# Optimization experiments

Hardware: AMD Instinct MI355X
Metric: run time of the kernel (lower is better)

## Reference

```python
import jax, jax.numpy as jnp
import numpy as np

B, S, D = 64, 14, 2048   # batch, enc_image_size, encoder_dim
A, H, E = 512, 512, 512  # attention_dim, lstm_size, embedding_size
V, L = 10000, 20         # vocab_size, max caption length (T = L-1 decode steps)


def setup_inputs() -> dict:
    key = jax.random.key(0)
    ks = jax.random.split(key, 24)
    p = lambda k, shape: jax.random.normal(k, shape, jnp.float32) * 0.02
    features = jax.random.normal(ks[0], (B, S, S, D), jnp.float32)
    captions = jax.random.randint(ks[1], (B, L), 0, V)
    # sorted descending lengths in [2, L], max forced to L so T_dec = L-1
    lengths = jnp.sort(jax.random.randint(ks[2], (B,), 2, L + 1))[::-1]
    lengths = lengths.at[0].set(L)
    return {
        'features': features, 'captions': captions, 'lengths': lengths,
        'emb': p(ks[3], (V, E)),
        'W_ih': p(ks[4], (4 * H, D + E)), 'b_ih': p(ks[5], (4 * H,)),
        'W_hh': p(ks[6], (4 * H, H)), 'b_hh': p(ks[7], (4 * H,)),
        'h_fc_w': p(ks[8], (H, D)), 'h_fc_b': p(ks[9], (H,)),
        'c_fc_w': p(ks[10], (H, D)), 'c_fc_b': p(ks[11], (H,)),
        'f_beta_w': p(ks[12], (D, H)), 'f_beta_b': p(ks[13], (D,)),
        'cls_w': p(ks[14], (V, H)), 'cls_b': p(ks[15], (V,)),
        'enc_w': p(ks[16], (A, D)), 'enc_b': p(ks[17], (A,)),
        'dec_w': p(ks[18], (A, H)), 'dec_b': p(ks[19], (A,)),
        'att_w': p(ks[20], (1, A)), 'att_b': p(ks[21], (1,)),
    }


def reference(features, captions, lengths, emb, W_ih, b_ih, W_hh, b_hh,
              h_fc_w, h_fc_b, c_fc_w, c_fc_b, f_beta_w, f_beta_b,
              cls_w, cls_b, enc_w, enc_b, dec_w, dec_b, att_w, att_b):
    feats = features.reshape(features.shape[0], -1, features.shape[-1])  # (B,P,D)
    emb_seq = emb[captions]                                              # (B,L,E)
    mean_f = feats.mean(axis=1)
    h = mean_f @ h_fc_w.T + h_fc_b
    c = mean_f @ c_fc_w.T + c_fc_b
    dec_len = lengths - 1
    T = captions.shape[1] - 1
    # attention encoder projection is time-invariant: hoist out of the loop
    att1 = jnp.einsum('bpd,ad->bpa', feats, enc_w) + enc_b               # (B,P,A)

    def step(carry, xs):
        h, c = carry
        x_emb, t = xs
        att2 = h @ dec_w.T + dec_b                                       # (B,A)
        e = jnp.einsum('bpa,a->bp', jax.nn.relu(att1 + att2[:, None, :]), att_w[0]) + att_b[0]
        alpha = jax.nn.softmax(e, axis=1)                                # (B,P)
        awe = jnp.einsum('bp,bpd->bd', alpha, feats)
        gate = jax.nn.sigmoid(h @ f_beta_w.T + f_beta_b)
        awe = gate * awe
        x = jnp.concatenate([x_emb, awe], axis=1)                        # (B,E+D)
        gates = x @ W_ih.T + b_ih + h @ W_hh.T + b_hh                    # torch gate order i,f,g,o
        i, f, g, o = jnp.split(gates, 4, axis=1)
        c2 = jax.nn.sigmoid(f) * c + jax.nn.sigmoid(i) * jnp.tanh(g)
        h2 = jax.nn.sigmoid(o) * jnp.tanh(c2)
        y = h2 @ cls_w.T + cls_b                                         # dropout = eval identity
        active = (t < dec_len)[:, None]
        return (h2, c2), (jnp.where(active, y, 0.0), jnp.where(active, alpha, 0.0))

    xs = (jnp.swapaxes(emb_seq[:, :T], 0, 1), jnp.arange(T))
    (_, _), (y_pred, alphas) = jax.lax.scan(step, (h, c), xs)
    return jnp.swapaxes(y_pred, 0, 1), jnp.swapaxes(alphas, 0, 1)
```

## Files before the change

kernel.cpp:

```cpp
#include <hip/hip_runtime.h>
#include <math.h>

typedef __attribute__((ext_vector_type(8))) short bf16x8;
typedef __attribute__((ext_vector_type(8))) unsigned short u16x8;
typedef __attribute__((ext_vector_type(4))) float f32x4;

#define NB 64
#define NP 196
#define ND 2048
#define NA 512
#define NH 512
#define NE 512
#define NV 10000
#define NT 19
#define NKX 3072
#define NROW (NB*NP)
#define NVP 10112
#define MROW 1280
#define PP 200

__device__ __forceinline__ unsigned short f2bu(float f){
    unsigned int u; __builtin_memcpy(&u, &f, 4);
    u = (u + 0x7FFFu + ((u >> 16) & 1u)) >> 16;
    return (unsigned short)u;
}
__device__ __forceinline__ float b2f(short s){
    unsigned int u = ((unsigned int)(unsigned short)s) << 16;
    float f; __builtin_memcpy(&f, &u, 4); return f;
}
__device__ __forceinline__ float sigm(float x){ return 1.f/(1.f + __expf(-x)); }

__device__ __forceinline__ void gll16(const void* g, void* l){
    __builtin_amdgcn_global_load_lds(
        (const __attribute__((address_space(1))) void*)g,
        (__attribute__((address_space(3))) void*)l, 16, 0, 0);
}


__global__ void k_cast4(const float4* __restrict__ src, ushort4* __restrict__ dst, int n4){
    int stride = gridDim.x * blockDim.x;
    for (int i = blockIdx.x*blockDim.x + threadIdx.x; i < n4; i += stride){
        float4 v = src[i];
        ushort4 o = { f2bu(v.x), f2bu(v.y), f2bu(v.z), f2bu(v.w) };
        dst[i] = o;
    }
}

__global__ void k_wcat(const float* __restrict__ wih, const float* __restrict__ whh,
                       unsigned short* __restrict__ wcat){
    int j = blockIdx.x;
    int k = blockIdx.y*256 + threadIdx.x;
    float v = (k < 2560) ? wih[j*2560 + k] : whh[j*512 + (k - 2560)];
    wcat[j*NKX + k] = f2bu(v);
}

__global__ void k_tr(const float* __restrict__ feats,
                     unsigned short* __restrict__ fbf,
                     unsigned short* __restrict__ ftr,
                     float* __restrict__ meanf){
    __shared__ unsigned short sm[64][202];
    __shared__ float rsum[256];
    int dt = blockIdx.x;
    int b  = blockIdx.y;
    int tid = threadIdx.x;
    int d = tid & 63;
    int gd = dt*64 + d;
    float s = 0.f;
    for (int p = (tid >> 6); p < NP; p += 4){
        float v = feats[((size_t)(b*NP + p))*ND + gd];
        unsigned short u = f2bu(v);
        fbf[((size_t)(b*NP + p))*ND + gd] = u;
        sm[d][p] = u;
        s += v;
    }
    rsum[tid] = s;
    __syncthreads();
    if (tid < 64)
        meanf[b*ND + dt*64 + tid] =
            (rsum[tid] + rsum[tid+64] + rsum[tid+128] + rsum[tid+192]) * (1.f/196.f);
    for (int v = tid; v < 64*25; v += 256){
        int r = v/25, c = v - r*25;
        u16x8 o;
        #pragma unroll
        for (int j = 0; j < 8; j++){ int p = c*8 + j; o[j] = (p < NP) ? sm[r][p] : (unsigned short)0; }
        *(u16x8*)(ftr + ((size_t)(b*ND + dt*64 + r))*PP + c*8) = o;
    }
}

__global__ void k_hc0(const float* __restrict__ meanf,
                      const float* __restrict__ hw, const float* __restrict__ hb,
                      const float* __restrict__ cw, const float* __restrict__ cb,
                      unsigned short* __restrict__ hbf, float* __restrict__ cst){
    int sel = blockIdx.y;
    const float* wmat = sel ? cw : hw;
    const float* bias = sel ? cb : hb;
    int jg = blockIdx.x;
    int tid = threadIdx.x;
    int b = tid & 63, jj = tid >> 6;
    int j = jg*4 + jj;
    __shared__ float ml[64][33];
    __shared__ float wl[4][32];
    float acc = 0.f;
    for (int kc = 0; kc < ND; kc += 32){
        __syncthreads();
        #pragma unroll
        for (int q = 0; q < 8; q++){
            int lin = tid + q*256;
            int r = lin >> 5, kk = lin & 31;
            ml[r][kk] = meanf[r*ND + kc + kk];
        }
        if (tid < 128){ int r = tid >> 5, kk = tid & 31; wl[r][kk] = wmat[(jg*4 + r)*ND + kc + kk]; }
        __syncthreads();
        #pragma unroll
        for (int kk = 0; kk < 32; kk++) acc += ml[b][kk] * wl[jj][kk];
    }
    acc += bias[j];
    if (sel) cst[b*NH + j] = acc;
    else     hbf[b*NH + j] = f2bu(acc);
}

template<int K>
__device__ __forceinline__ void gemm128(const unsigned short* __restrict__ A,
                                        const unsigned short* __restrict__ B,
                                        int brow, int bcol, f32x4 acc[4][4]){
    __shared__ unsigned short As[128*32];
    __shared__ unsigned short Bs[128*32];
    int tid = threadIdx.x;
    int w = tid >> 6, l = tid & 63;
    int wr = (w >> 1) * 64, wc = (w & 1) * 64;
    int lr = l & 15, kg = (l >> 4) * 8;
    const unsigned short* ga0 = A + (size_t)(brow + (tid >> 2))*K + (tid & 3)*8;
    const unsigned short* gb0 = B + (size_t)(bcol + (tid >> 2))*K + (tid & 3)*8;
    for (int k0 = 0; k0 < K; k0 += 32){
        __syncthreads();
        gll16(ga0 + k0,            As + w*512);
        gll16(ga0 + (size_t)64*K + k0, As + 2048 + w*512);
        gll16(gb0 + k0,            Bs + w*512);
        gll16(gb0 + (size_t)64*K + k0, Bs + 2048 + w*512);
        __syncthreads();
        bf16x8 af[4], bfr[4];
        #pragma unroll
        for (int mi = 0; mi < 4; mi++)
            af[mi] = *(const bf16x8*)(As + (wr + mi*16 + lr)*32 + kg);
        #pragma unroll
        for (int ni = 0; ni < 4; ni++)
            bfr[ni] = *(const bf16x8*)(Bs + (wc + ni*16 + lr)*32 + kg);
        #pragma unroll
        for (int ni = 0; ni < 4; ni++){
            #pragma unroll
            for (int mi = 0; mi < 4; mi++)
                acc[mi][ni] = __builtin_amdgcn_mfma_f32_16x16x32_bf16(af[mi], bfr[ni], acc[mi][ni], 0, 0, 0);
        }
    }
}

__global__ void k_gemm_att1(const unsigned short* __restrict__ fbf,
                            const unsigned short* __restrict__ encw,
                            const float* __restrict__ enc_b,
                            unsigned short* __restrict__ att1){
    f32x4 acc[4][4] = {};
    int brow = blockIdx.x*128, bcol = blockIdx.y*128;
    gemm128<ND>(fbf, encw, brow, bcol, acc);
    int w = threadIdx.x >> 6, l = threadIdx.x & 63;
    int wr = (w >> 1) * 64, wc = (w & 1) * 64;
    int r0 = brow + wr + (l >> 4)*4;
    int c0 = bcol + wc + (l & 15);
    #pragma unroll
    for (int ni = 0; ni < 4; ni++){
        int col = c0 + ni*16;
        float eb = enc_b[col];
        #pragma unroll
        for (int mi = 0; mi < 4; mi++){
            #pragma unroll
            for (int r = 0; r < 4; r++)
                att1[(size_t)(r0 + mi*16 + r)*NA + col] = f2bu(acc[mi][ni][r] + eb);
        }
    }
}

__global__ void k_gemm_cls(const unsigned short* __restrict__ hsb,
                           const unsigned short* __restrict__ clsw,
                           const float* __restrict__ cls_b,
                           const int* __restrict__ lengths,
                           float* __restrict__ yout){
    f32x4 acc[4][4] = {};
    int brow = blockIdx.x*128, bcol = blockIdx.y*128;
    gemm128<NH>(hsb, clsw, brow, bcol, acc);
    int w = threadIdx.x >> 6, l = threadIdx.x & 63;
    int wr = (w >> 1) * 64, wc = (w & 1) * 64;
    int r0 = brow + wr + (l >> 4)*4;
    int c0 = bcol + wc + (l & 15);
    #pragma unroll
    for (int ni = 0; ni < 4; ni++){
        int col = c0 + ni*16;
        if (col >= NV) continue;
        float cb = cls_b[col];
        #pragma unroll
        for (int mi = 0; mi < 4; mi++){
            #pragma unroll
            for (int r = 0; r < 4; r++){
                int grow = r0 + mi*16 + r;
                if (grow >= NT*64) continue;
                int t = grow >> 6, bb = grow & 63;
                int active = t < (lengths[bb] - 1);
                yout[((size_t)bb*NT + t)*NV + col] = active ? (acc[mi][ni][r] + cb) : 0.f;
            }
        }
    }
}


__global__ void k_hproj(const unsigned short* __restrict__ hbf,
                        const unsigned short* __restrict__ hwb,
                        float* __restrict__ hp){
    int w = threadIdx.x >> 6, l = threadIdx.x & 63;
    int nt = blockIdx.x;
    int row = 16*w + (l & 15);
    int col = nt*16 + (l & 15);
    int kg = (l >> 4) * 8;
    f32x4 acc = {};
    for (int k0 = 0; k0 < NH; k0 += 32){
        bf16x8 af = *(const bf16x8*)(hbf + row*NH + k0 + kg);
        bf16x8 bv = *(const bf16x8*)(hwb + col*NH + k0 + kg);
        acc = __builtin_amdgcn_mfma_f32_16x16x32_bf16(af, bv, acc, 0, 0, 0);
    }
    int r0 = 16*w + (l >> 4)*4;
    #pragma unroll
    for (int r = 0; r < 4; r++)
        hp[(r0 + r)*2560 + col] = acc[r];
}

__global__ void k_e(const unsigned short* __restrict__ att1,
                    const float* __restrict__ hp, const float* __restrict__ dec_b,
                    const float* __restrict__ att_w, const float* __restrict__ att_b,
                    const float* __restrict__ emb, const int* __restrict__ captions,
                    const unsigned short* __restrict__ hbf,
                    unsigned short* __restrict__ xh, float* __restrict__ ews, int t){
    __shared__ float at2[NA];
    __shared__ float aw[NA];
    int b = blockIdx.x >> 2, pc = blockIdx.x & 3;
    int tid = threadIdx.x;
    for (int j = tid; j < NA; j += 256){
        at2[j] = hp[b*2560 + j] + dec_b[j];
        aw[j]  = att_w[j];
    }
    if (pc == 0){
        int cap = captions[b*20 + t];
        for (int k = tid; k < NE; k += 256) xh[b*NKX + k] = f2bu(emb[cap*NE + k]);
        for (int j = tid; j < NH; j += 256) xh[b*NKX + 2560 + j] = hbf[b*NH + j];
    }
    __syncthreads();
    int pl = tid >> 2, q = tid & 3;
    if (pl < 49){
        int p = pc*49 + pl;
        const unsigned short* arow = att1 + ((size_t)(b*NP + p))*NA + q*128;
        float s = 0.f;
        for (int a0 = 0; a0 < 128; a0 += 8){
            bf16x8 v = *(const bf16x8*)(arow + a0);
            #pragma unroll
            for (int e = 0; e < 8; e++){
                int a = q*128 + a0 + e;
                float x = b2f(v[e]) + at2[a];
                s += fmaxf(x, 0.f) * aw[a];
            }
        }
        s += __shfl_xor(s, 1);
        s += __shfl_xor(s, 2);
        if (q == 0) ews[b*NP + p] = s + att_b[0];
    }
}

__global__ void k_awe(const float* __restrict__ ews, const unsigned short* __restrict__ ftr,
                      const float* __restrict__ hp, const float* __restrict__ f_beta_b,
                      const int* __restrict__ lengths,
                      unsigned short* __restrict__ xh, float* __restrict__ alphas_out, int t){
    __shared__ float al[PP];
    __shared__ float red[256];
    int dc = blockIdx.x;
    int b  = blockIdx.y;
    int tid = threadIdx.x;
    float v = (tid < NP) ? ews[b*NP + tid] : -1e30f;
    red[tid] = v; __syncthreads();
    for (int s = 128; s > 0; s >>= 1){ if (tid < s) red[tid] = fmaxf(red[tid], red[tid+s]); __syncthreads(); }
    float m = red[0]; __syncthreads();
    float ev = (tid < NP) ? __expf(v - m) : 0.f;
    red[tid] = ev; __syncthreads();
    for (int s = 128; s > 0; s >>= 1){ if (tid < s) red[tid] += red[tid+s]; __syncthreads(); }
    float inv = 1.f / red[0];
    if (tid < NP) al[tid] = ev * inv;
    if (tid >= NP && tid < PP) al[tid] = 0.f;
    __syncthreads();
    if (dc == 0 && tid < NP){
        int active = t < (lengths[b] - 1);
        alphas_out[((size_t)b*NT + t)*NP + tid] = active ? al[tid] : 0.f;
    }
    int d = dc*256 + tid;
    const unsigned short* fr = ftr + ((size_t)(b*ND + d))*PP;
    float a0 = 0.f, a1 = 0.f, a2 = 0.f, a3 = 0.f;
    #pragma unroll
    for (int c = 0; c < 25; c++){
        bf16x8 vv = *(const bf16x8*)(fr + c*8);
        float* accp = (c & 3) == 0 ? &a0 : (c & 3) == 1 ? &a1 : (c & 3) == 2 ? &a2 : &a3;
        float s = 0.f;
        #pragma unroll
        for (int j = 0; j < 8; j++) s += al[c*8 + j] * b2f(vv[j]);
        *accp += s;
    }
    float acc = (a0 + a1) + (a2 + a3);
    float g = sigm(hp[b*2560 + 512 + d] + f_beta_b[d]);
    xh[b*NKX + 512 + d] = f2bu(g * acc);
}

__global__ void k_gates(const unsigned short* __restrict__ xh,
                        const unsigned short* __restrict__ wcat,
                        float* __restrict__ part){
    int w = threadIdx.x >> 6, l = threadIdx.x & 63;
    int nt = blockIdx.x;
    int s  = blockIdx.y;
    int row = 16*w + (l & 15);
    int col = nt*16 + (l & 15);
    int kg = (l >> 4) * 8;
    int kbase = s*384;
    f32x4 acc = {};
    for (int k0 = 0; k0 < 384; k0 += 32){
        bf16x8 af = *(const bf16x8*)(xh + row*NKX + kbase + k0 + kg);
        bf16x8 bv = *(const bf16x8*)(wcat + col*NKX + kbase + k0 + kg);
        acc = __builtin_amdgcn_mfma_f32_16x16x32_bf16(af, bv, acc, 0, 0, 0);
    }
    int r0 = 16*w + (l >> 4)*4;
    #pragma unroll
    for (int r = 0; r < 4; r++)
        part[(s*64 + r0 + r)*2048 + col] = acc[r];
}

__global__ void k_lstm(const float* __restrict__ part,
                       const float* __restrict__ b_ih, const float* __restrict__ b_hh,
                       float* __restrict__ cst, unsigned short* __restrict__ hbf,
                       unsigned short* __restrict__ hsb, int t){
    int idx = blockIdx.x*256 + threadIdx.x;
    int b = idx >> 9, j = idx & 511;
    float gi = b_ih[j]        + b_hh[j];
    float gf = b_ih[512 + j]  + b_hh[512 + j];
    float gg = b_ih[1024 + j] + b_hh[1024 + j];
    float go = b_ih[1536 + j] + b_hh[1536 + j];
    #pragma unroll
    for (int s = 0; s < 8; s++){
        const float* pb = part + (s*64 + b)*2048;
        gi += pb[j]; gf += pb[512 + j]; gg += pb[1024 + j]; go += pb[1536 + j];
    }
    float c = cst[b*NH + j];
    float c2 = sigm(gf)*c + sigm(gi)*tanhf(gg);
    float h2 = sigm(go)*tanhf(c2);
    cst[b*NH + j] = c2;
    unsigned short hb16 = f2bu(h2);
    hbf[b*NH + j] = hb16;
    hsb[((t - 1)*64 + b)*NH + j] = hb16;
}


extern "C" void kernel_launch(void* const* d_in, const int* in_sizes, int n_in,
                              void* d_out, int out_size, void* d_ws, size_t ws_size,
                              hipStream_t stream){
    const float* features = (const float*)d_in[0];
    const int*   captions = (const int*)d_in[1];
    const int*   lengths  = (const int*)d_in[2];
    const float* emb      = (const float*)d_in[3];
    const float* W_ih     = (const float*)d_in[4];
    const float* b_ih     = (const float*)d_in[5];
    const float* W_hh     = (const float*)d_in[6];
    const float* b_hh     = (const float*)d_in[7];
    const float* h_fc_w   = (const float*)d_in[8];
    const float* h_fc_b   = (const float*)d_in[9];
    const float* c_fc_w   = (const float*)d_in[10];
    const float* c_fc_b   = (const float*)d_in[11];
    const float* f_beta_w = (const float*)d_in[12];
    const float* f_beta_b = (const float*)d_in[13];
    const float* cls_w    = (const float*)d_in[14];
    const float* cls_b    = (const float*)d_in[15];
    const float* enc_w    = (const float*)d_in[16];
    const float* enc_b    = (const float*)d_in[17];
    const float* dec_w    = (const float*)d_in[18];
    const float* dec_b    = (const float*)d_in[19];
    const float* att_w    = (const float*)d_in[20];
    const float* att_b    = (const float*)d_in[21];

    char* w = (char*)d_ws;
    size_t off = 0;
    auto alloc = [&](size_t bytes)->char*{
        char* p = w + off;
        off += (bytes + 255) & ~(size_t)255;
        return p;
    };
    unsigned short* fbf   = (unsigned short*)alloc((size_t)NROW*ND*2);
    unsigned short* ftr   = (unsigned short*)alloc((size_t)NB*ND*PP*2);
    unsigned short* att1  = (unsigned short*)alloc((size_t)NROW*NA*2);
    unsigned short* encwb = (unsigned short*)alloc((size_t)NA*ND*2);
    unsigned short* hwb   = (unsigned short*)alloc((size_t)2560*NH*2);
    unsigned short* wcat  = (unsigned short*)alloc((size_t)2048*NKX*2);
    unsigned short* clswb = (unsigned short*)alloc((size_t)NVP*NH*2);
    unsigned short* hsb   = (unsigned short*)alloc((size_t)MROW*NH*2);
    unsigned short* hbf   = (unsigned short*)alloc((size_t)64*NH*2);
    unsigned short* xh    = (unsigned short*)alloc((size_t)64*NKX*2);
    float* meanf = (float*)alloc((size_t)64*ND*4);
    float* cst   = (float*)alloc((size_t)64*NH*4);
    float* hp    = (float*)alloc((size_t)64*2560*4);
    float* ews   = (float*)alloc((size_t)64*NP*4);
    float* part  = (float*)alloc((size_t)8*64*2048*4);

    float* yout = (float*)d_out;
    float* alphas_out = yout + (size_t)NB*NT*NV;

    k_tr<<<dim3(32, 64), 256, 0, stream>>>(features, fbf, ftr, meanf);
    k_cast4<<<1024, 256, 0, stream>>>((const float4*)enc_w, (ushort4*)encwb, NA*ND/4);
    k_cast4<<<256, 256, 0, stream>>>((const float4*)dec_w, (ushort4*)hwb, 512*512/4);
    k_cast4<<<1024, 256, 0, stream>>>((const float4*)f_beta_w, (ushort4*)(hwb + 512*512), 2048*512/4);
    k_wcat<<<dim3(2048, 12), 256, 0, stream>>>(W_ih, W_hh, wcat);
    k_cast4<<<2048, 256, 0, stream>>>((const float4*)cls_w, (ushort4*)clswb, NV*NH/4);
    hipMemsetAsync(clswb + (size_t)NV*NH, 0, (size_t)(NVP - NV)*NH*2, stream);
    hipMemsetAsync(hsb + (size_t)NT*64*NH, 0, (size_t)(MROW - NT*64)*NH*2, stream);
    k_hc0<<<dim3(128, 2), 256, 0, stream>>>(meanf, h_fc_w, h_fc_b, c_fc_w, c_fc_b, hbf, cst);
    k_gemm_att1<<<dim3(98, 4), 256, 0, stream>>>(fbf, encwb, enc_b, att1);

    for (int t = 0; t < NT; t++){
        if (t > 0)
            k_lstm<<<128, 256, 0, stream>>>(part, b_ih, b_hh, cst, hbf, hsb, t);
        k_hproj<<<160, 256, 0, stream>>>(hbf, hwb, hp);
        k_e<<<256, 256, 0, stream>>>(att1, hp, dec_b, att_w, att_b, emb, captions, hbf, xh, ews, t);
        k_awe<<<dim3(8, 64), 256, 0, stream>>>(ews, ftr, hp, f_beta_b, lengths, xh, alphas_out, t);
        k_gates<<<dim3(128, 8), 256, 0, stream>>>(xh, wcat, part);
    }
    k_lstm<<<128, 256, 0, stream>>>(part, b_ih, b_hh, cst, hbf, hsb, NT);
    k_gemm_cls<<<dim3(10, 79), 256, 0, stream>>>(hsb, clswb, cls_b, lengths, yout);
}
```

Measured before the change: 1.236 ms.

## Hoist embedding gate GEMM, fuse weight casts, vectorize transpose and use MFMA init

The embedding contribution to the LSTM gates (with both biases folded in) becomes one batched GEMM over all timesteps before the loop, so the per-step gate GEMM only covers the attention-weighted features and hidden state. All weight casts and pad memsets are merged into a single prep kernel. The feature transpose/cast kernel is rewritten to use float4 loads with a two-stage mean reduction. The initial h/c projection now uses bf16 MFMA instead of a scalar fp32 loop. This trims per-step work and launch count, at the cost of extra buffers and bf16 rounding of the mean features.

```diff
diff --git a/kernel.cpp b/kernel.cpp
--- a/kernel.cpp
+++ b/kernel.cpp
@@ -13,7 +13,6 @@
 #define NE 512
 #define NV 10000
 #define NT 19
-#define NKX 3072
 #define NROW (NB*NP)
 #define NVP 10112
 #define MROW 1280
@@ -24,8 +23,8 @@
     u = (u + 0x7FFFu + ((u >> 16) & 1u)) >> 16;
     return (unsigned short)u;
 }
-__device__ __forceinline__ float b2f(short s){
-    unsigned int u = ((unsigned int)(unsigned short)s) << 16;
+__device__ __forceinline__ float b2f(unsigned short s){
+    unsigned int u = ((unsigned int)s) << 16;
     float f; __builtin_memcpy(&f, &u, 4); return f;
 }
 __device__ __forceinline__ float sigm(float x){ return 1.f/(1.f + __expf(-x)); }
@@ -37,86 +36,172 @@
 }
 
 
-__global__ void k_cast4(const float4* __restrict__ src, ushort4* __restrict__ dst, int n4){
-    int stride = gridDim.x * blockDim.x;
-    for (int i = blockIdx.x*blockDim.x + threadIdx.x; i < n4; i += stride){
-        float4 v = src[i];
-        ushort4 o = { f2bu(v.x), f2bu(v.y), f2bu(v.z), f2bu(v.w) };
-        dst[i] = o;
-    }
-}
-
-__global__ void k_wcat(const float* __restrict__ wih, const float* __restrict__ whh,
-                       unsigned short* __restrict__ wcat){
-    int j = blockIdx.x;
-    int k = blockIdx.y*256 + threadIdx.x;
-    float v = (k < 2560) ? wih[j*2560 + k] : whh[j*512 + (k - 2560)];
-    wcat[j*NKX + k] = f2bu(v);
-}
-
-__global__ void k_tr(const float* __restrict__ feats,
-                     unsigned short* __restrict__ fbf,
-                     unsigned short* __restrict__ ftr,
-                     float* __restrict__ meanf){
-    __shared__ unsigned short sm[64][202];
-    __shared__ float rsum[256];
-    int dt = blockIdx.x;
+__global__ void k_prep(const float4* __restrict__ enc_w, const float4* __restrict__ dec_w,
+                       const float4* __restrict__ f_beta_w, const float4* __restrict__ W_ih,
+                       const float4* __restrict__ W_hh, const float4* __restrict__ h_fc_w,
+                       const float4* __restrict__ c_fc_w, const float4* __restrict__ cls_w,
+                       ushort4* __restrict__ encwb, ushort4* __restrict__ whp,
+                       ushort4* __restrict__ wgates, ushort4* __restrict__ wembb,
+                       ushort4* __restrict__ whc, ushort4* __restrict__ clswb,
+                       ushort4* __restrict__ hsb_pad){
+    const int n0 = NA*ND/4;
+    const int n1 = 2560*512/4;
+    const int n2 = 2048*2560/4;
+    const int n3 = 2048*512/4;
+    const int n4 = 1024*2048/4;
+    const int n5 = NVP*NH/4;
+    const int n6 = 64*512/4;
+    const int total = n0+n1+n2+n3+n4+n5+n6;
+    int stride = gridDim.x*blockDim.x;
+    for (int i = blockIdx.x*blockDim.x + threadIdx.x; i < total; i += stride){
+        int idx = i;
+        float4 v; ushort4 o;
+        if (idx < n0){
+            v = enc_w[idx];
+            o.x = f2bu(v.x); o.y = f2bu(v.y); o.z = f2bu(v.z); o.w = f2bu(v.w);
+            encwb[idx] = o; continue;
+        }
+        idx -= n0;
+        if (idx < n1){
+            v = (idx < 512*512/4) ? dec_w[idx] : f_beta_w[idx - 512*512/4];
+            o.x = f2bu(v.x); o.y = f2bu(v.y); o.z = f2bu(v.z); o.w = f2bu(v.w);
+            whp[idx] = o; continue;
+        }
+        idx -= n1;
+        if (idx < n2){
+            int j = idx / 640, kk4 = idx - j*640;
+            v = (kk4 < 512) ? W_ih[(size_t)j*640 + 128 + kk4] : W_hh[(size_t)j*128 + (kk4 - 512)];
+            o.x = f2bu(v.x); o.y = f2bu(v.y); o.z = f2bu(v.z); o.w = f2bu(v.w);
+            wgates[idx] = o; continue;
+        }
+        idx -= n2;
+        if (idx < n3){
+            int j = idx >> 7, kk4 = idx & 127;
+            v = W_ih[(size_t)j*640 + kk4];
+            o.x = f2bu(v.x); o.y = f2bu(v.y); o.z = f2bu(v.z); o.w = f2bu(v.w);
+            wembb[idx] = o; continue;
+        }
+        idx -= n3;
+        if (idx < n4){
+            v = (idx < 512*2048/4) ? h_fc_w[idx] : c_fc_w[idx - 512*2048/4];
+            o.x = f2bu(v.x); o.y = f2bu(v.y); o.z = f2bu(v.z); o.w = f2bu(v.w);
+            whc[idx] = o; continue;
+        }
+        idx -= n4;
+        if (idx < n5){
+            if (idx < NV*NH/4){
+                v = cls_w[idx];
+                o.x = f2bu(v.x); o.y = f2bu(v.y); o.z = f2bu(v.z); o.w = f2bu(v.w);
+            } else { o.x = 0; o.y = 0; o.z = 0; o.w = 0; }
+            clswb[idx] = o; continue;
+        }
+        idx -= n5;
+        o.x = 0; o.y = 0; o.z = 0; o.w = 0;
+        hsb_pad[idx] = o;
+    }
+}
+
+__global__ void k_tr3(const float* __restrict__ feats,
+                      unsigned short* __restrict__ fbf,
+                      unsigned short* __restrict__ ftr,
+                      float* __restrict__ mp){
+    __shared__ unsigned short sm[64][260];
+    __shared__ float4 msum[256];
+    int dc = blockIdx.x;
     int b  = blockIdx.y;
+    int ph = blockIdx.z;
     int tid = threadIdx.x;
-    int d = tid & 63;
-    int gd = dt*64 + d;
-    float s = 0.f;
-    for (int p = (tid >> 6); p < NP; p += 4){
-        float v = feats[((size_t)(b*NP + p))*ND + gd];
-        unsigned short u = f2bu(v);
-        fbf[((size_t)(b*NP + p))*ND + gd] = u;
-        sm[d][p] = u;
-        s += v;
-    }
-    rsum[tid] = s;
+    int c4 = tid & 63;
+    int rq = tid >> 6;
+    int D0 = dc*256;
+    float4 acc = {0.f,0.f,0.f,0.f};
+    for (int pcl = 0; pcl < 2; pcl++){
+        int pc = ph*2 + pcl;
+        __syncthreads();
+        #pragma unroll
+        for (int i = 0; i < 16; i++){
+            int rl = rq + 4*i;
+            int p = pc*64 + rl;
+            float4 v = {0.f,0.f,0.f,0.f};
+            if (p < NP) v = *(const float4*)(feats + ((size_t)(b*NP + p))*ND + D0 + c4*4);
+            acc.x += v.x; acc.y += v.y; acc.z += v.z; acc.w += v.w;
+            ushort4 u4;
+            u4.x = f2bu(v.x); u4.y = f2bu(v.y); u4.z = f2bu(v.z); u4.w = f2bu(v.w);
+            if (p < NP) *(ushort4*)(fbf + ((size_t)(b*NP + p))*ND + D0 + c4*4) = u4;
+            *(ushort4*)&sm[rl][c4*4] = u4;
+        }
+        __syncthreads();
+        int gmax = (pc == 3) ? 1 : 8;
+        for (int g = 0; g < gmax; g++){
+            u16x8 o;
+            #pragma unroll
+            for (int k = 0; k < 8; k++) o[k] = sm[g*8 + k][tid];
+            *(u16x8*)(ftr + ((size_t)(b*ND + D0 + tid))*PP + pc*64 + g*8) = o;
+        }
+    }
+    msum[tid] = acc;
     __syncthreads();
-    if (tid < 64)
-        meanf[b*ND + dt*64 + tid] =
-            (rsum[tid] + rsum[tid+64] + rsum[tid+128] + rsum[tid+192]) * (1.f/196.f);
-    for (int v = tid; v < 64*25; v += 256){
-        int r = v/25, c = v - r*25;
-        u16x8 o;
-        #pragma unroll
-        for (int j = 0; j < 8; j++){ int p = c*8 + j; o[j] = (p < NP) ? sm[r][p] : (unsigned short)0; }
-        *(u16x8*)(ftr + ((size_t)(b*ND + dt*64 + r))*PP + c*8) = o;
-    }
-}
-
-__global__ void k_hc0(const float* __restrict__ meanf,
-                      const float* __restrict__ hw, const float* __restrict__ hb,
-                      const float* __restrict__ cw, const float* __restrict__ cb,
-                      unsigned short* __restrict__ hbf, float* __restrict__ cst){
-    int sel = blockIdx.y;
-    const float* wmat = sel ? cw : hw;
-    const float* bias = sel ? cb : hb;
-    int jg = blockIdx.x;
+    if (tid < 64){
+        float4 s0 = msum[tid], s1 = msum[tid+64], s2 = msum[tid+128], s3 = msum[tid+192];
+        float4 tot = { (s0.x+s1.x)+(s2.x+s3.x), (s0.y+s1.y)+(s2.y+s3.y),
+                       (s0.z+s1.z)+(s2.z+s3.z), (s0.w+s1.w)+(s2.w+s3.w) };
+        *(float4*)(mp + ((size_t)ph*64 + b)*ND + D0 + tid*4) = tot;
+    }
+}
+
+__global__ void k_mean2(const float* __restrict__ mp, unsigned short* __restrict__ meanbf){
+    int i = blockIdx.x*1024 + threadIdx.x*4;
+    float4 a = *(const float4*)(mp + i);
+    float4 b = *(const float4*)(mp + 64*ND + i);
+    ushort4 o;
+    o.x = f2bu((a.x+b.x)*(1.f/196.f)); o.y = f2bu((a.y+b.y)*(1.f/196.f));
+    o.z = f2bu((a.z+b.z)*(1.f/196.f)); o.w = f2bu((a.w+b.w)*(1.f/196.f));
+    *(ushort4*)(meanbf + i) = o;
+}
+
+__global__ void k_embg(const float* __restrict__ emb, const int* __restrict__ captions,
+                       unsigned short* __restrict__ embcat){
+    int blk = blockIdx.x, tid = threadIdx.x;
+    int r = blk*4 + (tid >> 6);
+    int cg = tid & 63;
+    u16x8 o;
+    #pragma unroll
+    for (int k = 0; k < 8; k++) o[k] = 0;
+    if (r < NT*64){
+        int t = r >> 6, b = r & 63;
+        int tok = captions[b*20 + t];
+        const float* e = emb + (size_t)tok*NE + cg*8;
+        float4 v0 = *(const float4*)e;
+        float4 v1 = *(const float4*)(e + 4);
+        o[0] = f2bu(v0.x); o[1] = f2bu(v0.y); o[2] = f2bu(v0.z); o[3] = f2bu(v0.w);
+        o[4] = f2bu(v1.x); o[5] = f2bu(v1.y); o[6] = f2bu(v1.z); o[7] = f2bu(v1.w);
+    }
+    *(u16x8*)(embcat + (size_t)r*NE + cg*8) = o;
+}
+
+__global__ void k_hc0m(const unsigned short* __restrict__ meanbf,
+                       const unsigned short* __restrict__ whc,
+                       const float* __restrict__ h_fc_b, const float* __restrict__ c_fc_b,
+                       unsigned short* __restrict__ hbf, float* __restrict__ cst){
     int tid = threadIdx.x;
-    int b = tid & 63, jj = tid >> 6;
-    int j = jg*4 + jj;
-    __shared__ float ml[64][33];
-    __shared__ float wl[4][32];
-    float acc = 0.f;
-    for (int kc = 0; kc < ND; kc += 32){
-        __syncthreads();
-        #pragma unroll
-        for (int q = 0; q < 8; q++){
-            int lin = tid + q*256;
-            int r = lin >> 5, kk = lin & 31;
-            ml[r][kk] = meanf[r*ND + kc + kk];
-        }
-        if (tid < 128){ int r = tid >> 5, kk = tid & 31; wl[r][kk] = wmat[(jg*4 + r)*ND + kc + kk]; }
-        __syncthreads();
-        #pragma unroll
-        for (int kk = 0; kk < 32; kk++) acc += ml[b][kk] * wl[jj][kk];
-    }
-    acc += bias[j];
-    if (sel) cst[b*NH + j] = acc;
-    else     hbf[b*NH + j] = f2bu(acc);
+    int w = tid >> 6, l = tid & 63;
+    int nt = blockIdx.x;
+    int row = 16*w + (l & 15);
+    int col = nt*16 + (l & 15);
+    int kg = (l >> 4) * 8;
+    f32x4 acc = {};
+    for (int k0 = 0; k0 < ND; k0 += 32){
+        bf16x8 af = *(const bf16x8*)(meanbf + (size_t)row*ND + k0 + kg);
+        bf16x8 bv = *(const bf16x8*)(whc + (size_t)col*ND + k0 + kg);
+        acc = __builtin_amdgcn_mfma_f32_16x16x32_bf16(af, bv, acc, 0, 0, 0);
+    }
+    int r0 = 16*w + (l >> 4)*4;
+    #pragma unroll
+    for (int r = 0; r < 4; r++){
+        int b = r0 + r;
+        if (col < 512) hbf[b*NH + col] = f2bu(acc[r] + h_fc_b[col]);
+        else           cst[b*NH + (col - 512)] = acc[r] + c_fc_b[col - 512];
+    }
 }
 
 template<int K>
@@ -133,9 +218,9 @@
     const unsigned short* gb0 = B + (size_t)(bcol + (tid >> 2))*K + (tid & 3)*8;
     for (int k0 = 0; k0 < K; k0 += 32){
         __syncthreads();
-        gll16(ga0 + k0,            As + w*512);
+        gll16(ga0 + k0,                As + w*512);
         gll16(ga0 + (size_t)64*K + k0, As + 2048 + w*512);
-        gll16(gb0 + k0,            Bs + w*512);
+        gll16(gb0 + k0,                Bs + w*512);
         gll16(gb0 + (size_t)64*K + k0, Bs + 2048 + w*512);
         __syncthreads();
         bf16x8 af[4], bfr[4];
@@ -174,6 +259,30 @@
             #pragma unroll
             for (int r = 0; r < 4; r++)
                 att1[(size_t)(r0 + mi*16 + r)*NA + col] = f2bu(acc[mi][ni][r] + eb);
+        }
+    }
+}
+
+__global__ void k_gemb(const unsigned short* __restrict__ embcat,
+                       const unsigned short* __restrict__ wembb,
+                       const float* __restrict__ b_ih, const float* __restrict__ b_hh,
+                       float* __restrict__ gemb){
+    f32x4 acc[4][4] = {};
+    int brow = blockIdx.x*128, bcol = blockIdx.y*128;
+    gemm128<NE>(embcat, wembb, brow, bcol, acc);
+    int w = threadIdx.x >> 6, l = threadIdx.x & 63;
+    int wr = (w >> 1) * 64, wc = (w & 1) * 64;
+    int r0 = brow + wr + (l >> 4)*4;
+    int c0 = bcol + wc + (l & 15);
+    #pragma unroll
+    for (int ni = 0; ni < 4; ni++){
+        int col = c0 + ni*16;
+        float bias = b_ih[col] + b_hh[col];
+        #pragma unroll
+        for (int mi = 0; mi < 4; mi++){
+            #pragma unroll
+            for (int r = 0; r < 4; r++)
+                gemb[(size_t)(r0 + mi*16 + r)*2048 + col] = acc[mi][ni][r] + bias;
         }
     }
 }
@@ -210,8 +319,30 @@
 }
 
 
+__global__ void k_lstm(const float* __restrict__ part, const float* __restrict__ gemb,
+                       float* __restrict__ cst, unsigned short* __restrict__ hbf,
+                       unsigned short* __restrict__ hsb, int t){
+    int idx = blockIdx.x*256 + threadIdx.x;
+    int b = idx >> 9, j = idx & 511;
+    const float* ge = gemb + ((size_t)(t - 1)*64 + b)*2048;
+    float gi = ge[j], gf = ge[512 + j], gg = ge[1024 + j], go = ge[1536 + j];
+    #pragma unroll
+    for (int s = 0; s < 10; s++){
+        const float* pb = part + (size_t)(s*64 + b)*2048;
+        gi += pb[j]; gf += pb[512 + j]; gg += pb[1024 + j]; go += pb[1536 + j];
+    }
+    float c = cst[b*NH + j];
+    float c2 = sigm(gf)*c + sigm(gi)*tanhf(gg);
+    float h2 = sigm(go)*tanhf(c2);
+    cst[b*NH + j] = c2;
+    unsigned short u = f2bu(h2);
+    hbf[b*NH + j] = u;
+    hsb[((size_t)(t - 1)*64 + b)*NH + j] = u;
+}
+
 __global__ void k_hproj(const unsigned short* __restrict__ hbf,
-                        const unsigned short* __restrict__ hwb,
+                        const unsigned short* __restrict__ whp,
+                        const float* __restrict__ dec_b, const float* __restrict__ f_beta_b,
                         float* __restrict__ hp){
     int w = threadIdx.x >> 6, l = threadIdx.x & 63;
     int nt = blockIdx.x;
@@ -221,33 +352,27 @@
     f32x4 acc = {};
     for (int k0 = 0; k0 < NH; k0 += 32){
         bf16x8 af = *(const bf16x8*)(hbf + row*NH + k0 + kg);
-        bf16x8 bv = *(const bf16x8*)(hwb + col*NH + k0 + kg);
+        bf16x8 bv = *(const bf16x8*)(whp + (size_t)col*NH + k0 + kg);
         acc = __builtin_amdgcn_mfma_f32_16x16x32_bf16(af, bv, acc, 0, 0, 0);
     }
     int r0 = 16*w + (l >> 4)*4;
+    float bias = (col < 512) ? dec_b[col] : f_beta_b[col - 512];
     #pragma unroll
     for (int r = 0; r < 4; r++)
-        hp[(r0 + r)*2560 + col] = acc[r];
+        hp[(r0 + r)*2560 + col] = acc[r] + bias;
 }
 
 __global__ void k_e(const unsigned short* __restrict__ att1,
-                    const float* __restrict__ hp, const float* __restrict__ dec_b,
+                    const float* __restrict__ hp,
                     const float* __restrict__ att_w, const float* __restrict__ att_b,
-                    const float* __restrict__ emb, const int* __restrict__ captions,
-                    const unsigned short* __restrict__ hbf,
-                    unsigned short* __restrict__ xh, float* __restrict__ ews, int t){
+                    float* __restrict__ ews){
     __shared__ float at2[NA];
     __shared__ float aw[NA];
     int b = blockIdx.x >> 2, pc = blockIdx.x & 3;
     int tid = threadIdx.x;
     for (int j = tid; j < NA; j += 256){
-        at2[j] = hp[b*2560 + j] + dec_b[j];
+        at2[j] = hp[b*2560 + j];
         aw[j]  = att_w[j];
-    }
-    if (pc == 0){
-        int cap = captions[b*20 + t];
-        for (int k = tid; k < NE; k += 256) xh[b*NKX + k] = f2bu(emb[cap*NE + k]);
-        for (int j = tid; j < NH; j += 256) xh[b*NKX + 2560 + j] = hbf[b*NH + j];
     }
     __syncthreads();
     int pl = tid >> 2, q = tid & 3;
@@ -259,9 +384,9 @@
             bf16x8 v = *(const bf16x8*)(arow + a0);
             #pragma unroll
             for (int e = 0; e < 8; e++){
-                int a = q*128 + a0 + e;
-                float x = b2f(v[e]) + at2[a];
-                s += fmaxf(x, 0.f) * aw[a];
+                int ai = q*128 + a0 + e;
+                float x = b2f((unsigned short)v[e]) + at2[ai];
+                s += fmaxf(x, 0.f) * aw[ai];
             }
         }
         s += __shfl_xor(s, 1);
@@ -271,9 +396,8 @@
 }
 
 __global__ void k_awe(const float* __restrict__ ews, const unsigned short* __restrict__ ftr,
-                      const float* __restrict__ hp, const float* __restrict__ f_beta_b,
-                      const int* __restrict__ lengths,
-                      unsigned short* __restrict__ xh, float* __restrict__ alphas_out, int t){
+                      const float* __restrict__ hp, const int* __restrict__ lengths,
+                      unsigned short* __restrict__ xg, float* __restrict__ alphas, int t){
     __shared__ float al[PP];
     __shared__ float red[256];
     int dc = blockIdx.x;
@@ -292,7 +416,7 @@
     __syncthreads();
     if (dc == 0 && tid < NP){
         int active = t < (lengths[b] - 1);
-        alphas_out[((size_t)b*NT + t)*NP + tid] = active ? al[tid] : 0.f;
+        alphas[((size_t)b*NT + t)*NP + tid] = active ? al[tid] : 0.f;
     }
     int d = dc*256 + tid;
     const unsigned short* fr = ftr + ((size_t)(b*ND + d))*PP;
@@ -300,61 +424,57 @@
     #pragma unroll
     for (int c = 0; c < 25; c++){
         bf16x8 vv = *(const bf16x8*)(fr + c*8);
-        float* accp = (c & 3) == 0 ? &a0 : (c & 3) == 1 ? &a1 : (c & 3) == 2 ? &a2 : &a3;
-        float s = 0.f;
-        #pragma unroll
-        for (int j = 0; j < 8; j++) s += al[c*8 + j] * b2f(vv[j]);
-        *accp += s;
-    }
-    float acc = (a0 + a1) + (a2 + a3);
-    float g = sigm(hp[b*2560 + 512 + d] + f_beta_b[d]);
-    xh[b*NKX + 512 + d] = f2bu(g * acc);
-}
-
-__global__ void k_gates(const unsigned short* __restrict__ xh,
-                        const unsigned short* __restrict__ wcat,
+        float ss = 0.f;
+        #pragma unroll
+        for (int j = 0; j < 8; j++) ss += al[c*8 + j] * b2f((unsigned short)vv[j]);
+        if ((c & 3) == 0) a0 += ss; else if ((c & 3) == 1) a1 += ss;
+        else if ((c & 3) == 2) a2 += ss; else a3 += ss;
+    }
+    float accv = (a0 + a1) + (a2 + a3);
+    float g = sigm(hp[b*2560 + 512 + d]);
+    xg[b*2048 + d] = f2bu(g * accv);
+}
+
+__global__ void k_gates(const unsigned short* __restrict__ xg,
+                        const unsigned short* __restrict__ hbf,
+                        const unsigned short* __restrict__ wgates,
                         float* __restrict__ part){
-    int w = threadIdx.x >> 6, l = threadIdx.x & 63;
     int nt = blockIdx.x;
     int s  = blockIdx.y;
+    int w = threadIdx.x >> 6, l = threadIdx.x & 63;
     int row = 16*w + (l & 15);
     int col = nt*16 + (l & 15);
     int kg = (l >> 4) * 8;
-    int kbase = s*384;
+    const unsigned short* arow = (s < 8) ? (xg + row*2048 + s*256)
+                                         : (hbf + row*512 + (s - 8)*256);
+    const unsigned short* brow = wgates + (size_t)col*2560 + s*256;
     f32x4 acc = {};
-    for (int k0 = 0; k0 < 384; k0 += 32){
-        bf16x8 af = *(const bf16x8*)(xh + row*NKX + kbase + k0 + kg);
-        bf16x8 bv = *(const bf16x8*)(wcat + col*NKX + kbase + k0 + kg);
+    for (int k0 = 0; k0 < 256; k0 += 32){
+        bf16x8 af = *(const bf16x8*)(arow + k0 + kg);
+        bf16x8 bv = *(const bf16x8*)(brow + k0 + kg);
         acc = __builtin_amdgcn_mfma_f32_16x16x32_bf16(af, bv, acc, 0, 0, 0);
     }
     int r0 = 16*w + (l >> 4)*4;
     #pragma unroll
     for (int r = 0; r < 4; r++)
-        part[(s*64 + r0 + r)*2048 + col] = acc[r];
-}
-
-__global__ void k_lstm(const float* __restrict__ part,
-                       const float* __restrict__ b_ih, const float* __restrict__ b_hh,
-                       float* __restrict__ cst, unsigned short* __restrict__ hbf,
-                       unsigned short* __restrict__ hsb, int t){
+        part[(size_t)(s*64 + r0 + r)*2048 + col] = acc[r];
+}
+
+__global__ void k_lstm_fin(const float* __restrict__ part, const float* __restrict__ gemb,
+                           const float* __restrict__ cst, unsigned short* __restrict__ hsb){
     int idx = blockIdx.x*256 + threadIdx.x;
     int b = idx >> 9, j = idx & 511;
-    float gi = b_ih[j]        + b_hh[j];
-    float gf = b_ih[512 + j]  + b_hh[512 + j];
-    float gg = b_ih[1024 + j] + b_hh[1024 + j];
-    float go = b_ih[1536 + j] + b_hh[1536 + j];
-    #pragma unroll
-    for (int s = 0; s < 8; s++){
-        const float* pb = part + (s*64 + b)*2048;
+    const float* ge = gemb + ((size_t)(NT - 1)*64 + b)*2048;
+    float gi = ge[j], gf = ge[512 + j], gg = ge[1024 + j], go = ge[1536 + j];
+    #pragma unroll
+    for (int s = 0; s < 10; s++){
+        const float* pb = part + (size_t)(s*64 + b)*2048;
         gi += pb[j]; gf += pb[512 + j]; gg += pb[1024 + j]; go += pb[1536 + j];
     }
     float c = cst[b*NH + j];
     float c2 = sigm(gf)*c + sigm(gi)*tanhf(gg);
     float h2 = sigm(go)*tanhf(c2);
-    cst[b*NH + j] = c2;
-    unsigned short hb16 = f2bu(h2);
-    hbf[b*NH + j] = hb16;
-    hsb[((t - 1)*64 + b)*NH + j] = hb16;
+    hsb[((size_t)(NT - 1)*64 + b)*NH + j] = f2bu(h2);
 }
 
 
@@ -391,44 +511,52 @@
         off += (bytes + 255) & ~(size_t)255;
         return p;
     };
-    unsigned short* fbf   = (unsigned short*)alloc((size_t)NROW*ND*2);
-    unsigned short* ftr   = (unsigned short*)alloc((size_t)NB*ND*PP*2);
-    unsigned short* att1  = (unsigned short*)alloc((size_t)NROW*NA*2);
-    unsigned short* encwb = (unsigned short*)alloc((size_t)NA*ND*2);
-    unsigned short* hwb   = (unsigned short*)alloc((size_t)2560*NH*2);
-    unsigned short* wcat  = (unsigned short*)alloc((size_t)2048*NKX*2);
-    unsigned short* clswb = (unsigned short*)alloc((size_t)NVP*NH*2);
-    unsigned short* hsb   = (unsigned short*)alloc((size_t)MROW*NH*2);
-    unsigned short* hbf   = (unsigned short*)alloc((size_t)64*NH*2);
-    unsigned short* xh    = (unsigned short*)alloc((size_t)64*NKX*2);
-    float* meanf = (float*)alloc((size_t)64*ND*4);
+    unsigned short* fbf    = (unsigned short*)alloc((size_t)NROW*ND*2);
+    unsigned short* ftr    = (unsigned short*)alloc((size_t)NB*ND*PP*2);
+    unsigned short* att1   = (unsigned short*)alloc((size_t)NROW*NA*2);
+    unsigned short* encwb  = (unsigned short*)alloc((size_t)NA*ND*2);
+    unsigned short* whp    = (unsigned short*)alloc((size_t)2560*NH*2);
+    unsigned short* wgates = (unsigned short*)alloc((size_t)2048*2560*2);
+    unsigned short* wembb  = (unsigned short*)alloc((size_t)2048*NE*2);
+    unsigned short* whc    = (unsigned short*)alloc((size_t)1024*ND*2);
+    unsigned short* clswb  = (unsigned short*)alloc((size_t)NVP*NH*2);
+    unsigned short* embcat = (unsigned short*)alloc((size_t)MROW*NE*2);
+    unsigned short* hsb    = (unsigned short*)alloc((size_t)MROW*NH*2);
+    unsigned short* hbf    = (unsigned short*)alloc((size_t)64*NH*2);
+    unsigned short* xg     = (unsigned short*)alloc((size_t)64*2048*2);
+    unsigned short* meanbf = (unsigned short*)alloc((size_t)64*ND*2);
+    float* mp    = (float*)alloc((size_t)2*64*ND*4);
+    float* gemb  = (float*)alloc((size_t)MROW*2048*4);
     float* cst   = (float*)alloc((size_t)64*NH*4);
     float* hp    = (float*)alloc((size_t)64*2560*4);
     float* ews   = (float*)alloc((size_t)64*NP*4);
-    float* part  = (float*)alloc((size_t)8*64*2048*4);
+    float* part  = (float*)alloc((size_t)10*64*2048*4);
 
     float* yout = (float*)d_out;
     float* alphas_out = yout + (size_t)NB*NT*NV;
 
-    k_tr<<<dim3(32, 64), 256, 0, stream>>>(features, fbf, ftr, meanf);
-    k_cast4<<<1024, 256, 0, stream>>>((const float4*)enc_w, (ushort4*)encwb, NA*ND/4);
-    k_cast4<<<256, 256, 0, stream>>>((const float4*)dec_w, (ushort4*)hwb, 512*512/4);
-    k_cast4<<<1024, 256, 0, stream>>>((const float4*)f_beta_w, (ushort4*)(hwb + 512*512), 2048*512/4);
-    k_wcat<<<dim3(2048, 12), 256, 0, stream>>>(W_ih, W_hh, wcat);
-    k_cast4<<<2048, 256, 0, stream>>>((const float4*)cls_w, (ushort4*)clswb, NV*NH/4);
-    hipMemsetAsync(clswb + (size_t)NV*NH, 0, (size_t)(NVP - NV)*NH*2, stream);
-    hipMemsetAsync(hsb + (size_t)NT*64*NH, 0, (size_t)(MROW - NT*64)*NH*2, stream);
-    k_hc0<<<dim3(128, 2), 256, 0, stream>>>(meanf, h_fc_w, h_fc_b, c_fc_w, c_fc_b, hbf, cst);
+    k_tr3<<<dim3(8, 64, 2), 256, 0, stream>>>(features, fbf, ftr, mp);
+    k_prep<<<2048, 256, 0, stream>>>((const float4*)enc_w, (const float4*)dec_w,
+                                     (const float4*)f_beta_w, (const float4*)W_ih,
+                                     (const float4*)W_hh, (const float4*)h_fc_w,
+                                     (const float4*)c_fc_w, (const float4*)cls_w,
+                                     (ushort4*)encwb, (ushort4*)whp, (ushort4*)wgates,
+                                     (ushort4*)wembb, (ushort4*)whc, (ushort4*)clswb,
+                                     (ushort4*)(hsb + (size_t)NT*64*NH));
+    k_embg<<<320, 256, 0, stream>>>(emb, captions, embcat);
+    k_mean2<<<128, 256, 0, stream>>>(mp, meanbf);
+    k_hc0m<<<64, 256, 0, stream>>>(meanbf, whc, h_fc_b, c_fc_b, hbf, cst);
     k_gemm_att1<<<dim3(98, 4), 256, 0, stream>>>(fbf, encwb, enc_b, att1);
+    k_gemb<<<dim3(10, 16), 256, 0, stream>>>(embcat, wembb, b_ih, b_hh, gemb);
 
     for (int t = 0; t < NT; t++){
         if (t > 0)
-            k_lstm<<<128, 256, 0, stream>>>(part, b_ih, b_hh, cst, hbf, hsb, t);
-        k_hproj<<<160, 256, 0, stream>>>(hbf, hwb, hp);
-        k_e<<<256, 256, 0, stream>>>(att1, hp, dec_b, att_w, att_b, emb, captions, hbf, xh, ews, t);
-        k_awe<<<dim3(8, 64), 256, 0, stream>>>(ews, ftr, hp, f_beta_b, lengths, xh, alphas_out, t);
-        k_gates<<<dim3(128, 8), 256, 0, stream>>>(xh, wcat, part);
-    }
-    k_lstm<<<128, 256, 0, stream>>>(part, b_ih, b_hh, cst, hbf, hsb, NT);
+            k_lstm<<<128, 256, 0, stream>>>(part, gemb, cst, hbf, hsb, t);
+        k_hproj<<<160, 256, 0, stream>>>(hbf, whp, dec_b, f_beta_b, hp);
+        k_e<<<256, 256, 0, stream>>>(att1, hp, att_w, att_b, ews);
+        k_awe<<<dim3(8, 64), 256, 0, stream>>>(ews, ftr, hp, lengths, xg, alphas_out, t);
+        k_gates<<<dim3(128, 10), 256, 0, stream>>>(xg, hbf, wgates, part);
+    }
+    k_lstm_fin<<<128, 256, 0, stream>>>(part, gemb, cst, hsb);
     k_gemm_cls<<<dim3(10, 79), 256, 0, stream>>>(hsb, clswb, cls_b, lengths, yout);
 }
```

Result: faster. 1.125 ms (-9.0%).
